# Kernel tuning notes

Measured on AMD Instinct MI355X. Metric: run time of the kernel, lower is better.

The kernel has to match this reference:

```python
import jax, jax.numpy as jnp
import numpy as np

B, S, HID = 2, 2048, 2048
NH, NOPE, ROPE = 16, 128, 64
HD = NOPE + ROPE          # 192
VHD = 128
KVR, QR = 512, 1536
FFN = 5632
THETA = 10000.0
EPS = 1e-6


def rmsnorm(x, w, eps=EPS):
    xf = x.astype(jnp.float32)
    rms = jnp.sqrt(jnp.mean(xf * xf, axis=-1, keepdims=True) + eps)
    return (xf / rms).astype(x.dtype) * w


def apply_rope(x, cos, sin):
    # x: (..., rope_dim); half-split rotation convention
    half = x.shape[-1] // 2
    x1, x2 = x[..., :half], x[..., half:]
    return jnp.concatenate([x1 * cos - x2 * sin, x2 * cos + x1 * sin], axis=-1)


def rope_tables(seq_len, dim, theta=THETA):
    inv_freq = 1.0 / (theta ** (jnp.arange(0, dim, 2, dtype=jnp.float32) / dim))
    t = jnp.arange(seq_len, dtype=jnp.float32)
    freqs = jnp.outer(t, inv_freq)           # (S, dim/2)
    return jnp.cos(freqs), jnp.sin(freqs)


def setup_inputs():
    key = jax.random.key(0)
    ks = jax.random.split(key, 10)
    def w(k, shape, fan_in):
        return jax.random.normal(k, shape, dtype=jnp.float32) * (fan_in ** -0.5)
    return {
        'x': jax.random.normal(ks[0], (B, S, HID), dtype=jnp.float32),
        'attn_norm_w': jnp.ones((HID,), jnp.float32),
        'wq_down': w(ks[1], (HID, QR), HID),
        'wq_up': w(ks[2], (QR, NH * HD), QR),
        'wkv_down': w(ks[3], (HID, KVR + ROPE), HID),
        'kv_norm_w': jnp.ones((KVR,), jnp.float32),
        'wkv_up': w(ks[4], (KVR, NH * (NOPE + VHD)), KVR),
        'wout': w(ks[5], (NH * VHD, HID), NH * VHD),
        'ffn_norm_w': jnp.ones((HID,), jnp.float32),
        'w_gate': w(ks[6], (HID, FFN), HID),
        'w_up': w(ks[7], (HID, FFN), HID),
        'w_down': w(ks[8], (FFN, HID), FFN),
    }


def reference(x, attn_norm_w, wq_down, wq_up, wkv_down, kv_norm_w, wkv_up, wout,
              ffn_norm_w, w_gate, w_up, w_down):
    scale = 1.0 / np.sqrt(HD)
    # --- attention sub-block ---
    h = rmsnorm(x, attn_norm_w)
    q = (h @ wq_down) @ wq_up                       # (B,S,NH*HD)
    q = q.reshape(B, S, NH, HD)
    q_nope, q_rope = q[..., :NOPE], q[..., NOPE:]
    kv_full = h @ wkv_down                          # (B,S,KVR+ROPE)
    kv_c, k_rope = kv_full[..., :KVR], kv_full[..., KVR:]
    kv_c = rmsnorm(kv_c, kv_norm_w)
    kv_exp = (kv_c @ wkv_up).reshape(B, S, NH, NOPE + VHD)
    k_nope, v = kv_exp[..., :NOPE], kv_exp[..., NOPE:]

    cos, sin = rope_tables(S, ROPE)                 # (S, ROPE/2)
    cos4, sin4 = cos[None, :, None, :], sin[None, :, None, :]
    q_rope = apply_rope(q_rope, cos4, sin4)         # (B,S,NH,ROPE)
    k_rope = apply_rope(k_rope[:, :, None, :], cos4, sin4)  # (B,S,1,ROPE)
    k_rope = jnp.broadcast_to(k_rope, (B, S, NH, ROPE))

    q_full = jnp.concatenate([q_nope, q_rope], axis=-1)     # (B,S,NH,HD)
    k = jnp.concatenate([k_nope, k_rope], axis=-1)          # (B,S,NH,HD)

    scores = jnp.einsum('bqhd,bkhd->bhqk', q_full, k) * scale
    causal = jnp.tril(jnp.ones((S, S), dtype=bool))
    scores = jnp.where(causal[None, None], scores, jnp.finfo(scores.dtype).min)
    probs = jax.nn.softmax(scores, axis=-1)
    attn = jnp.einsum('bhqk,bkhd->bqhd', probs, v).reshape(B, S, NH * VHD)
    x = x + attn @ wout

    # --- SwiGLU MLP sub-block ---
    h2 = rmsnorm(x, ffn_norm_w)
    ffn = (jax.nn.silu(h2 @ w_gate) * (h2 @ w_up)) @ w_down
    return x + ffn
```

## Files before the change

### kernel.cpp

```cpp
#include <hip/hip_runtime.h>
#include <hip/hip_bf16.h>


using bf16x8 = __attribute__((ext_vector_type(8))) short;
using f32x4  = __attribute__((ext_vector_type(4))) float;

#define GLOBAL_AS __attribute__((address_space(1)))
#define LDS_AS    __attribute__((address_space(3)))
#define MFMA16(a, b, c) __builtin_amdgcn_mfma_f32_16x16x32_bf16((a), (b), (c), 0, 0, 0)

static constexpr int Sc = 2048;

__device__ __forceinline__ void gload16(const void* g, void* l) {
  __builtin_amdgcn_global_load_lds((const GLOBAL_AS unsigned int*)g,
                                   (LDS_AS unsigned int*)l, 16, 0, 0);
}
__device__ __forceinline__ float bf2f(unsigned short u) {
  union { float f; unsigned int i; } x; x.i = ((unsigned int)u) << 16; return x.f;
}
__device__ __forceinline__ unsigned short f2bf(float f) {
  union { float f; unsigned int i; } x; x.f = f;
  unsigned int i = x.i;
  return (unsigned short)((i + 0x7fffu + ((i >> 16) & 1u)) >> 16);
}
__device__ __forceinline__ int swz4(int r) { return ((r >> 2) & 3) ^ (r & 3); }

__global__ void fill_k(float* out, float v, int n) {
  int i = blockIdx.x * 256 + threadIdx.x;
  if (i < n) out[i] = v;
}

__global__ __launch_bounds__(256) void wtrans(const float* __restrict__ W,
                                              unsigned short* __restrict__ WT,
                                              int K, int N) {
  __shared__ float t[32][33];
  const int n0 = blockIdx.x * 32, k0 = blockIdx.y * 32;
  const int tx = threadIdx.x & 31, ty = threadIdx.x >> 5;
#pragma unroll
  for (int i = 0; i < 4; ++i) {
    int k = k0 + ty + i * 8;
    int n = n0 + tx;
    t[ty + i * 8][tx] = (n < N) ? W[(size_t)k * N + n] : 0.0f;
  }
  __syncthreads();
#pragma unroll
  for (int i = 0; i < 4; ++i) {
    int n = n0 + ty + i * 8;
    int k = k0 + tx;
    WT[(size_t)n * K + k] = f2bf(t[tx][ty + i * 8]);
  }
}

__global__ void rope_tab(float* __restrict__ cosT, float* __restrict__ sinT) {
  int i = blockIdx.x * 256 + threadIdx.x;
  if (i >= Sc * 32) return;
  int s = i >> 5, j = i & 31;
  float inv = powf(10000.0f, -(float)j / 32.0f);
  float a = (float)s * inv;
  cosT[i] = cosf(a);
  sinT[i] = sinf(a);
}

__global__ __launch_bounds__(256) void rmsnorm_k(const float* __restrict__ in,
                                                 const float* __restrict__ w,
                                                 unsigned short* __restrict__ out,
                                                 int D, int istride, int ostride) {
  const int row = blockIdx.x;
  const float* x = in + (size_t)row * istride;
  float ss = 0.f;
  for (int c = threadIdx.x * 4; c < D; c += 1024) {
    const float4 v = *(const float4*)(x + c);
    ss += v.x * v.x + v.y * v.y + v.z * v.z + v.w * v.w;
  }
#pragma unroll
  for (int off = 1; off < 64; off <<= 1) ss += __shfl_xor(ss, off);
  __shared__ float part[4];
  if ((threadIdx.x & 63) == 0) part[threadIdx.x >> 6] = ss;
  __syncthreads();
  float tot = part[0] + part[1] + part[2] + part[3];
  float r = rsqrtf(tot / (float)D + 1e-6f);
  for (int c = threadIdx.x * 4; c < D; c += 1024) {
    const float4 v = *(const float4*)(x + c);
    ushort4 o;
    o.x = f2bf(v.x * r * w[c + 0]);
    o.y = f2bf(v.y * r * w[c + 1]);
    o.z = f2bf(v.z * r * w[c + 2]);
    o.w = f2bf(v.w * r * w[c + 3]);
    *(ushort4*)(out + (size_t)row * ostride + c) = o;
  }
}

enum { EPI_BF16 = 0, EPI_F32 = 1, EPI_ADDF32 = 2, EPI_SILU = 3 };

template <int BMW, int EPI>
__global__ __launch_bounds__(512, 2) void gemm_big(const unsigned short* __restrict__ A,
                                                   const unsigned short* __restrict__ BT,
                                                   void* __restrict__ Cp,
                                                   const float* __restrict__ resid,
                                                   const unsigned short* __restrict__ other,
                                                   int M, int N, int K) {
  constexpr int BM = 128 * BMW;
  constexpr int AL = 2 * BMW;
  constexpr int MF = 4 * BMW;
  __shared__ unsigned short ldsA[2][BM * 64];
  __shared__ unsigned short ldsB[2][256 * 64];

  const int tid = threadIdx.x;
  const int w = tid >> 6, lane = tid & 63;
  const int rl = lane & 15, gh = lane >> 4;
  const int wm = w >> 2, wn = w & 3;

  const int nwg = gridDim.x;
  const int orig = blockIdx.x;
  const int qq = nwg >> 3, rr = nwg & 7;
  const int xcd = orig & 7, lidx = orig >> 3;
  const int fswz = (xcd < rr ? xcd * (qq + 1) : rr * (qq + 1) + (xcd - rr) * qq) + lidx;
  const int MT = M / BM;
  const int m0 = (fswz % MT) * BM;
  const int n0 = (fswz / MT) * 256;

  const unsigned short* srcA[AL];
#pragma unroll
  for (int i = 0; i < AL; ++i) {
    int G = i * 512 + tid, r = G >> 3, sl = (G & 7) ^ (r & 7);
    srcA[i] = A + (size_t)(m0 + r) * K + sl * 8;
  }
  const unsigned short* srcB[4];
#pragma unroll
  for (int i = 0; i < 4; ++i) {
    int G = i * 512 + tid, r = G >> 3, sl = (G & 7) ^ (r & 7);
    srcB[i] = BT + (size_t)(n0 + r) * K + sl * 8;
  }

  auto STAGE = [&](int kt, int p) {
    const int ko = kt * 64;
#pragma unroll
    for (int i = 0; i < AL; ++i)
      gload16(srcA[i] + ko, &ldsA[p][(i * 512 + w * 64) * 8]);
#pragma unroll
    for (int i = 0; i < 4; ++i)
      gload16(srcB[i] + ko, &ldsB[p][(i * 512 + w * 64) * 8]);
  };

  f32x4 acc[MF][4] = {};
  const int nk = K >> 6;

  STAGE(0, 0);
  STAGE(1, 1);
  if constexpr (BMW == 2) asm volatile("s_waitcnt vmcnt(8)" ::: "memory");
  else                    asm volatile("s_waitcnt vmcnt(6)" ::: "memory");
  __builtin_amdgcn_s_barrier();
  __builtin_amdgcn_sched_barrier(0);

  for (int kt = 0; kt < nk; ++kt) {
    const int cur = kt & 1;
    const unsigned short* lA = &ldsA[cur][0];
    const unsigned short* lB = &ldsB[cur][0];
    bf16x8 a[MF][2], b[4][2];
#pragma unroll
    for (int mf = 0; mf < MF; ++mf)
#pragma unroll
      for (int ks = 0; ks < 2; ++ks) {
        const int row = wm * (64 * BMW) + mf * 16 + rl;
        a[mf][ks] = *(const bf16x8*)&lA[row * 64 + (((ks << 2) + gh) ^ (row & 7)) * 8];
      }
#pragma unroll
    for (int nf = 0; nf < 4; ++nf)
#pragma unroll
      for (int ks = 0; ks < 2; ++ks) {
        const int row = wn * 64 + nf * 16 + rl;
        b[nf][ks] = *(const bf16x8*)&lB[row * 64 + (((ks << 2) + gh) ^ (row & 7)) * 8];
      }
    asm volatile("s_waitcnt lgkmcnt(0)" ::: "memory");
    __builtin_amdgcn_sched_barrier(0);
    __builtin_amdgcn_s_barrier();
    __builtin_amdgcn_sched_barrier(0);
    STAGE((kt + 2 < nk) ? kt + 2 : kt, cur);
    __builtin_amdgcn_s_setprio(1);
#pragma unroll
    for (int ks = 0; ks < 2; ++ks)
#pragma unroll
      for (int mf = 0; mf < MF; ++mf)
#pragma unroll
        for (int nf = 0; nf < 4; ++nf)
          acc[mf][nf] = MFMA16(a[mf][ks], b[nf][ks], acc[mf][nf]);
    __builtin_amdgcn_s_setprio(0);
    __builtin_amdgcn_sched_barrier(0);
    if constexpr (BMW == 2) asm volatile("s_waitcnt vmcnt(8)" ::: "memory");
    else                    asm volatile("s_waitcnt vmcnt(6)" ::: "memory");
    __builtin_amdgcn_s_barrier();
    __builtin_amdgcn_sched_barrier(0);
  }

#pragma unroll
  for (int mf = 0; mf < MF; ++mf) {
#pragma unroll
    for (int nf = 0; nf < 4; ++nf) {
#pragma unroll
      for (int rg = 0; rg < 4; ++rg) {
        const int row = m0 + wm * (64 * BMW) + mf * 16 + gh * 4 + rg;
        const int col = n0 + wn * 64 + nf * 16 + rl;
        const size_t idx = (size_t)row * N + col;
        const float v = acc[mf][nf][rg];
        if constexpr (EPI == EPI_BF16) {
          ((unsigned short*)Cp)[idx] = f2bf(v);
        } else if constexpr (EPI == EPI_F32) {
          ((float*)Cp)[idx] = v;
        } else if constexpr (EPI == EPI_ADDF32) {
          ((float*)Cp)[idx] = v + resid[idx];
        } else {
          float gv = bf2f(other[idx]);
          float sg = gv / (1.f + __expf(-gv));
          ((unsigned short*)Cp)[idx] = f2bf(sg * v);
        }
      }
    }
  }
}

template <int EPI>
__global__ __launch_bounds__(256) void gemm_bt(const unsigned short* __restrict__ A,
                                               const unsigned short* __restrict__ BT,
                                               void* __restrict__ Cp,
                                               const float* __restrict__ resid,
                                               const unsigned short* __restrict__ other,
                                               int M, int N, int K) {
  __shared__ unsigned short ldsA[2][128 * 32];
  __shared__ unsigned short ldsB[2][128 * 32];
  const int tid = threadIdx.x;
  const int w = tid >> 6, lane = tid & 63;
  const int nwg = gridDim.x;
  const int orig = blockIdx.x;
  const int qq = nwg >> 3, rr = nwg & 7;
  const int xcd = orig & 7, lidx = orig >> 3;
  const int fswz = (xcd < rr ? xcd * (qq + 1) : rr * (qq + 1) + (xcd - rr) * qq) + lidx;
  const int m0 = (fswz & 31) * 128;
  const int n0 = (fswz >> 5) * 128;

  const int wm = (w >> 1) * 64, wn = (w & 1) * 64;
  const int rl = lane & 15, gsel = lane >> 4;

  const int p0 = w * 64 + lane;
  const int p1 = p0 + 256;
  const int r0 = p0 >> 2, r1 = p1 >> 2;
  const int g0 = (p0 & 3) ^ swz4(r0), g1 = (p1 & 3) ^ swz4(r1);
  const unsigned short* gA0 = A + (size_t)(m0 + r0) * K + g0 * 8;
  const unsigned short* gA1 = A + (size_t)(m0 + r1) * K + g1 * 8;
  const unsigned short* gB0 = BT + (size_t)(n0 + r0) * K + g0 * 8;
  const unsigned short* gB1 = BT + (size_t)(n0 + r1) * K + g1 * 8;
  const int dA0 = (w * 64) * 8, dA1 = dA0 + 2048;

  int aoff[4], boff[4];
#pragma unroll
  for (int i = 0; i < 4; ++i) {
    int ra = wm + i * 16 + rl;
    aoff[i] = ra * 32 + (gsel ^ swz4(ra)) * 8;
    int rb = wn + i * 16 + rl;
    boff[i] = rb * 32 + (gsel ^ swz4(rb)) * 8;
  }

  auto STAGE = [&](int kt, int p) {
    const int ko = kt * 32;
    gload16(gA0 + ko, &ldsA[p][dA0]);
    gload16(gA1 + ko, &ldsA[p][dA1]);
    gload16(gB0 + ko, &ldsB[p][dA0]);
    gload16(gB1 + ko, &ldsB[p][dA1]);
  };

  f32x4 acc[4][4] = {};
  const int nk = K >> 5;

  STAGE(0, 0);
  STAGE(1, 1);
  for (int kt = 0; kt < nk; ++kt) {
    asm volatile("s_waitcnt vmcnt(4)" ::: "memory");
    __builtin_amdgcn_s_barrier();
    __builtin_amdgcn_sched_barrier(0);
    const unsigned short* lA = &ldsA[kt & 1][0];
    const unsigned short* lB = &ldsB[kt & 1][0];
    bf16x8 a[4], b[4];
#pragma unroll
    for (int i = 0; i < 4; ++i) a[i] = *(const bf16x8*)&lA[aoff[i]];
#pragma unroll
    for (int i = 0; i < 4; ++i) b[i] = *(const bf16x8*)&lB[boff[i]];
    __builtin_amdgcn_s_setprio(1);
#pragma unroll
    for (int i = 0; i < 4; ++i)
#pragma unroll
      for (int j = 0; j < 4; ++j) acc[i][j] = MFMA16(a[i], b[j], acc[i][j]);
    __builtin_amdgcn_s_setprio(0);
    __builtin_amdgcn_sched_barrier(0);
    __builtin_amdgcn_s_barrier();
    const int nxt = (kt + 2 < nk) ? kt + 2 : nk - 1;
    STAGE(nxt, kt & 1);
  }

#pragma unroll
  for (int i = 0; i < 4; ++i) {
#pragma unroll
    for (int j = 0; j < 4; ++j) {
#pragma unroll
      for (int rg = 0; rg < 4; ++rg) {
        const int row = m0 + wm + i * 16 + gsel * 4 + rg;
        const int col = n0 + wn + j * 16 + rl;
        const size_t idx = (size_t)row * N + col;
        const float v = acc[i][j][rg];
        if constexpr (EPI == EPI_BF16) {
          ((unsigned short*)Cp)[idx] = f2bf(v);
        } else if constexpr (EPI == EPI_F32) {
          ((float*)Cp)[idx] = v;
        } else if constexpr (EPI == EPI_ADDF32) {
          ((float*)Cp)[idx] = v + resid[idx];
        } else {
          float gv = bf2f(other[idx]);
          float sg = gv / (1.f + __expf(-gv));
          ((unsigned short*)Cp)[idx] = f2bf(sg * v);
        }
      }
    }
  }
}

__global__ __launch_bounds__(256) void repack_q(const unsigned short* __restrict__ q,
                                                const float* __restrict__ cosT,
                                                const float* __restrict__ sinT,
                                                unsigned short* __restrict__ Qc) {
  const int row = blockIdx.x;
  const int b = row >> 11, s = row & 2047;
  const float scale = 0.07216878364870322f;
  const unsigned short* qr = q + (size_t)row * 3072;
  for (int i = threadIdx.x; i < 3072; i += 256) {
    int h = i / 192, d = i - h * 192;
    float v;
    if (d < 128) {
      v = bf2f(qr[h * 192 + d]);
    } else {
      int j = d - 128;
      int jj = j & 31;
      float x1 = bf2f(qr[h * 192 + 128 + jj]);
      float x2 = bf2f(qr[h * 192 + 160 + jj]);
      float c = cosT[s * 32 + jj], sn = sinT[s * 32 + jj];
      v = (j < 32) ? (x1 * c - x2 * sn) : (x2 * c + x1 * sn);
    }
    Qc[((size_t)(b * 16 + h) * Sc + s) * 192 + d] = f2bf(v * scale);
  }
}

__global__ __launch_bounds__(256) void repack_kv(const unsigned short* __restrict__ kvex,
                                                 const float* __restrict__ kvf,
                                                 const float* __restrict__ cosT,
                                                 const float* __restrict__ sinT,
                                                 unsigned short* __restrict__ Kc,
                                                 unsigned short* __restrict__ VT) {
  __shared__ unsigned short vt_lds[32][136];
  const int bid = blockIdx.x;
  const int st = bid & 63;
  const int h = (bid >> 6) & 15;
  const int b = bid >> 10;
  const int s0 = st * 32;
  const int tid = threadIdx.x;
  const size_t KcBase = (size_t)(b * 16 + h) * Sc;
  for (int i = tid; i < 32 * 32; i += 256) {
    int r = i >> 5, g = i & 31;
    uint4 vdat = *(const uint4*)(kvex + (size_t)(b * Sc + s0 + r) * 4096 + h * 256 + g * 8);
    if (g < 16) {
      *(uint4*)(Kc + (KcBase + s0 + r) * 192 + g * 8) = vdat;
    } else {
      *(uint4*)(&vt_lds[r][(g - 16) * 8]) = vdat;
    }
  }
  for (int i = tid; i < 32 * 64; i += 256) {
    int r = i >> 6, d = i & 63;
    int s = s0 + r;
    int jj = d & 31;
    const float* kvrow = kvf + (size_t)(b * Sc + s) * 640;
    float x1 = kvrow[512 + jj], x2 = kvrow[544 + jj];
    float c = cosT[s * 32 + jj], sn = sinT[s * 32 + jj];
    float v = (d < 32) ? (x1 * c - x2 * sn) : (x2 * c + x1 * sn);
    Kc[(KcBase + s) * 192 + 128 + d] = f2bf(v);
  }
  __syncthreads();
  const int f = tid >> 1, sh = (tid & 1) * 16;
  unsigned int vals[8];
#pragma unroll
  for (int k2 = 0; k2 < 8; ++k2) {
    unsigned int lo = vt_lds[sh + 2 * k2][f];
    unsigned int hi = vt_lds[sh + 2 * k2 + 1][f];
    vals[k2] = lo | (hi << 16);
  }
  unsigned short* dst = VT + ((size_t)(b * 16 + h) * 128 + f) * Sc + s0 + sh;
  ((uint4*)dst)[0] = make_uint4(vals[0], vals[1], vals[2], vals[3]);
  ((uint4*)dst)[1] = make_uint4(vals[4], vals[5], vals[6], vals[7]);
}

__global__ __launch_bounds__(256) void attn_k(const unsigned short* __restrict__ Qc,
                                              const unsigned short* __restrict__ Kc,
                                              const unsigned short* __restrict__ VT,
                                              unsigned short* __restrict__ Ob) {
  __shared__ unsigned short lds_k[2][32 * 192];
  __shared__ unsigned short lds_v[2][128 * 32];
  __shared__ __align__(16) unsigned short p_lds[4][16 * 40];
  const int tid = threadIdx.x, w = tid >> 6, lane = tid & 63;
  const int rl = lane & 15, gh = lane >> 4;
  const int bidx = blockIdx.x;
  const int bh = bidx & 31;
  const int qt = 31 - (bidx >> 5);
  const unsigned short* Qh = Qc + (size_t)bh * Sc * 192;
  const unsigned short* Kh = Kc + (size_t)bh * Sc * 192;
  const unsigned short* Vh = VT + (size_t)bh * 128 * Sc;
  const int qr0 = qt * 64 + w * 16;

  bf16x8 qf[6];
#pragma unroll
  for (int kk = 0; kk < 6; ++kk)
    qf[kk] = *(const bf16x8*)(Qh + (size_t)(qr0 + rl) * 192 + kk * 32 + gh * 8);

  f32x4 o[8] = {};
  float mrun[4] = {-1e30f, -1e30f, -1e30f, -1e30f};
  float srun[4] = {0.f, 0.f, 0.f, 0.f};

  int kr[3], kg[3];
#pragma unroll
  for (int j = 0; j < 3; ++j) {
    int pp = j * 256 + w * 64 + lane;
    int r = pp / 24, gq = pp - r * 24;
    kr[j] = r;
    kg[j] = (gq & ~7) | ((gq & 7) ^ (r & 7));
  }
  int vr[2], vg[2];
#pragma unroll
  for (int j = 0; j < 2; ++j) {
    int pp = j * 256 + w * 64 + lane;
    int r = pp >> 2;
    vr[j] = r;
    vg[j] = (pp & 3) ^ swz4(r);
  }

  auto STAGE = [&](int t, int b) {
    const int k0 = t * 32;
#pragma unroll
    for (int j = 0; j < 3; ++j)
      gload16(Kh + (size_t)(k0 + kr[j]) * 192 + kg[j] * 8,
              &lds_k[b][(j * 256 + w * 64) * 8]);
#pragma unroll
    for (int j = 0; j < 2; ++j)
      gload16(Vh + (size_t)vr[j] * Sc + k0 + vg[j] * 8,
              &lds_v[b][(j * 256 + w * 64) * 8]);
  };

  STAGE(0, 0);
  asm volatile("s_waitcnt vmcnt(0)" ::: "memory");
  __builtin_amdgcn_s_barrier();
  __builtin_amdgcn_sched_barrier(0);

  const int nt = 2 * qt + 2;
  int cur = 0;
  for (int t = 0; t < nt; ++t) {
    if (t + 1 < nt) STAGE(t + 1, cur ^ 1);
    const int k0 = t * 32;
    if (k0 <= qr0 + 15) {
      const unsigned short* lk = lds_k[cur];
      const unsigned short* lv = lds_v[cur];
      f32x4 s0 = {0.f, 0.f, 0.f, 0.f}, s1 = {0.f, 0.f, 0.f, 0.f};
      __builtin_amdgcn_s_setprio(1);
#pragma unroll
      for (int kk = 0; kk < 6; ++kk) {
        const int gq = kk * 4 + gh;
        const int ph0 = (gq & ~7) | ((gq & 7) ^ (rl & 7));
        bf16x8 kf0 = *(const bf16x8*)&lk[rl * 192 + ph0 * 8];
        s0 = MFMA16(qf[kk], kf0, s0);
        bf16x8 kf1 = *(const bf16x8*)&lk[(16 + rl) * 192 + ph0 * 8];
        s1 = MFMA16(qf[kk], kf1, s1);
      }
      __builtin_amdgcn_s_setprio(0);
      if (k0 + 31 > qr0) {
#pragma unroll
        for (int rg = 0; rg < 4; ++rg) {
          int qrow = qr0 + gh * 4 + rg;
          if (k0 + rl > qrow) s0[rg] = -1e30f;
          if (k0 + 16 + rl > qrow) s1[rg] = -1e30f;
        }
      }
      float al[4];
#pragma unroll
      for (int rg = 0; rg < 4; ++rg) {
        float v = fmaxf(s0[rg], s1[rg]);
        v = fmaxf(v, __shfl_xor(v, 1));
        v = fmaxf(v, __shfl_xor(v, 2));
        v = fmaxf(v, __shfl_xor(v, 4));
        v = fmaxf(v, __shfl_xor(v, 8));
        float mn = fmaxf(mrun[rg], v);
        al[rg] = __expf(mrun[rg] - mn);
        mrun[rg] = mn;
        float p0 = __expf(s0[rg] - mn), p1 = __expf(s1[rg] - mn);
        s0[rg] = p0;
        s1[rg] = p1;
        float rs = p0 + p1;
        rs += __shfl_xor(rs, 1);
        rs += __shfl_xor(rs, 2);
        rs += __shfl_xor(rs, 4);
        rs += __shfl_xor(rs, 8);
        srun[rg] = srun[rg] * al[rg] + rs;
      }
#pragma unroll
      for (int i = 0; i < 8; ++i)
#pragma unroll
        for (int rg = 0; rg < 4; ++rg) o[i][rg] *= al[rg];
      unsigned short* pw = p_lds[w];
#pragma unroll
      for (int rg = 0; rg < 4; ++rg) {
        pw[(gh * 4 + rg) * 40 + rl] = f2bf(s0[rg]);
        pw[(gh * 4 + rg) * 40 + 16 + rl] = f2bf(s1[rg]);
      }
      bf16x8 pa = *(const bf16x8*)&pw[rl * 40 + gh * 8];
      __builtin_amdgcn_s_setprio(1);
#pragma unroll
      for (int vf = 0; vf < 8; ++vf) {
        int r = vf * 16 + rl;
        bf16x8 vfr = *(const bf16x8*)&lv[r * 32 + (gh ^ swz4(r)) * 8];
        o[vf] = MFMA16(pa, vfr, o[vf]);
      }
      __builtin_amdgcn_s_setprio(0);
    }
    asm volatile("s_waitcnt vmcnt(0)" ::: "memory");
    __builtin_amdgcn_s_barrier();
    __builtin_amdgcn_sched_barrier(0);
    cur ^= 1;
  }
  const int b = bh >> 4, hh = bh & 15;
  float rd[4];
#pragma unroll
  for (int rg = 0; rg < 4; ++rg) rd[rg] = 1.f / srun[rg];
#pragma unroll
  for (int vf = 0; vf < 8; ++vf) {
#pragma unroll
    for (int rg = 0; rg < 4; ++rg) {
      int srow = qr0 + gh * 4 + rg;
      int col = hh * 128 + vf * 16 + rl;
      Ob[((size_t)(b * Sc) + srow) * 2048 + col] = f2bf(o[vf][rg] * rd[rg]);
    }
  }
}

extern "C" void kernel_launch(void* const* d_in, const int* in_sizes, int n_in,
                              void* d_out, int out_size, void* d_ws, size_t ws_size,
                              hipStream_t stream) {
  (void)in_sizes; (void)n_in;
  const float* x    = (const float*)d_in[0];
  const float* anw  = (const float*)d_in[1];
  const float* wqd  = (const float*)d_in[2];
  const float* wqu  = (const float*)d_in[3];
  const float* wkvd = (const float*)d_in[4];
  const float* kvnw = (const float*)d_in[5];
  const float* wkvu = (const float*)d_in[6];
  const float* wout = (const float*)d_in[7];
  const float* fnw  = (const float*)d_in[8];
  const float* wg   = (const float*)d_in[9];
  const float* wu   = (const float*)d_in[10];
  const float* wd   = (const float*)d_in[11];
  float* out = (float*)d_out;

  char* ws = (char*)d_ws;
  size_t off = 0;
  auto alloc = [&](size_t bytes) -> char* {
    char* p = ws + off;
    off += (bytes + 255) & ~(size_t)255;
    return p;
  };
  unsigned short* wslot = (unsigned short*)alloc(5632ull * 2048 * 2);
  float* cosT           = (float*)alloc(2048ull * 32 * 4);
  float* sinT           = (float*)alloc(2048ull * 32 * 4);
  unsigned short* hbuf  = (unsigned short*)alloc(4096ull * 2048 * 2);
  char* arena           = alloc(4096ull * 1536 * 2 + 4096ull * 3072 * 2);
  float* kvf            = (float*)alloc(4096ull * 640 * 4);
  unsigned short* kvn   = (unsigned short*)alloc(4096ull * 512 * 2);
  unsigned short* Qc    = (unsigned short*)alloc(32ull * 2048 * 192 * 2);
  unsigned short* Kc    = (unsigned short*)alloc(32ull * 2048 * 192 * 2);
  unsigned short* VTb   = (unsigned short*)alloc(32ull * 128 * 2048 * 2);
  const size_t NEED = off;

  if (ws_size < NEED) {
    fill_k<<<dim3((out_size + 255) / 256), dim3(256), 0, stream>>>(
        out, (float)(ws_size >> 20), out_size);
    return;
  }

  unsigned short* qd    = (unsigned short*)arena;
  unsigned short* q     = (unsigned short*)(arena + 4096ull * 1536 * 2);
  unsigned short* kvex  = (unsigned short*)arena;
  unsigned short* h     = hbuf;
  unsigned short* attnb = hbuf;
  unsigned short* h2    = hbuf;
  unsigned short* gbuf  = Qc;
  float* x2             = out;

  dim3 blk(256), blk512(512);
  rope_tab<<<dim3(256), blk, 0, stream>>>(cosT, sinT);
  rmsnorm_k<<<dim3(4096), blk, 0, stream>>>(x, anw, h, 2048, 2048, 2048);

  wtrans<<<dim3(48, 64), blk, 0, stream>>>(wqd, wslot, 2048, 1536);
  gemm_big<1, EPI_BF16><<<dim3(32 * 6), blk512, 0, stream>>>(h, wslot, qd, nullptr, nullptr, 4096, 1536, 2048);
  wtrans<<<dim3(96, 48), blk, 0, stream>>>(wqu, wslot, 1536, 3072);
  gemm_big<2, EPI_BF16><<<dim3(16 * 12), blk512, 0, stream>>>(qd, wslot, q, nullptr, nullptr, 4096, 3072, 1536);
  repack_q<<<dim3(4096), blk, 0, stream>>>(q, cosT, sinT, Qc);

  wtrans<<<dim3(20, 64), blk, 0, stream>>>(wkvd, wslot, 2048, 576);
  gemm_bt<EPI_F32><<<dim3(5 * 32), blk, 0, stream>>>(h, wslot, kvf, nullptr, nullptr, 4096, 640, 2048);
  rmsnorm_k<<<dim3(4096), blk, 0, stream>>>(kvf, kvnw, kvn, 512, 640, 512);
  wtrans<<<dim3(128, 16), blk, 0, stream>>>(wkvu, wslot, 512, 4096);
  gemm_big<2, EPI_BF16><<<dim3(16 * 16), blk512, 0, stream>>>(kvn, wslot, kvex, nullptr, nullptr, 4096, 4096, 512);
  repack_kv<<<dim3(2048), blk, 0, stream>>>(kvex, kvf, cosT, sinT, Kc, VTb);

  attn_k<<<dim3(1024), blk, 0, stream>>>(Qc, Kc, VTb, attnb);
  wtrans<<<dim3(64, 64), blk, 0, stream>>>(wout, wslot, 2048, 2048);
  gemm_big<1, EPI_ADDF32><<<dim3(32 * 8), blk512, 0, stream>>>(attnb, wslot, x2, x, nullptr, 4096, 2048, 2048);

  rmsnorm_k<<<dim3(4096), blk, 0, stream>>>(x2, fnw, h2, 2048, 2048, 2048);
  wtrans<<<dim3(176, 64), blk, 0, stream>>>(wg, wslot, 2048, 5632);
  gemm_big<2, EPI_BF16><<<dim3(16 * 22), blk512, 0, stream>>>(h2, wslot, gbuf, nullptr, nullptr, 4096, 5632, 2048);
  wtrans<<<dim3(176, 64), blk, 0, stream>>>(wu, wslot, 2048, 5632);
  gemm_big<2, EPI_SILU><<<dim3(16 * 22), blk512, 0, stream>>>(h2, wslot, gbuf, nullptr, gbuf, 4096, 5632, 2048);
  wtrans<<<dim3(64, 176), blk, 0, stream>>>(wd, wslot, 5632, 2048);
  gemm_big<1, EPI_ADDF32><<<dim3(32 * 8), blk512, 0, stream>>>(gbuf, wslot, out, x2, nullptr, 4096, 2048, 5632);
}
```

Measured before the change: 834.0 us.

## Enlarge attention tiles to 128 queries x 64 keys with lazy rescale; widen weight transpose stores

The attention kernel now runs 512 threads per block, covering 128 query rows and streaming 64-key K/V tiles with an 8-way XOR swizzle. This halves the number of barriers and staging steps per key and gives more reuse of each loaded K/V tile. Online softmax skips rescaling of the accumulator unless the new tile max exceeds the running max by more than 8, and the row-sum reduction is deferred to the end. The weight transpose kernel now handles 64 K-rows per block and writes packed pairs of bf16 as 32-bit stores. The bigger tiles raise LDS use, which may reduce occupancy, and the lazy rescale relies on exp staying within fp32/bf16 range.

```diff
diff --git a/kernel.cpp b/kernel.cpp
--- a/kernel.cpp
+++ b/kernel.cpp
@@ -33,11 +33,11 @@
 __global__ __launch_bounds__(256) void wtrans(const float* __restrict__ W,
                                               unsigned short* __restrict__ WT,
                                               int K, int N) {
-  __shared__ float t[32][33];
-  const int n0 = blockIdx.x * 32, k0 = blockIdx.y * 32;
+  __shared__ float t[64][33];
+  const int n0 = blockIdx.x * 32, k0 = blockIdx.y * 64;
   const int tx = threadIdx.x & 31, ty = threadIdx.x >> 5;
 #pragma unroll
-  for (int i = 0; i < 4; ++i) {
+  for (int i = 0; i < 8; ++i) {
     int k = k0 + ty + i * 8;
     int n = n0 + tx;
     t[ty + i * 8][tx] = (n < N) ? W[(size_t)k * N + n] : 0.0f;
@@ -45,9 +45,11 @@
   __syncthreads();
 #pragma unroll
   for (int i = 0; i < 4; ++i) {
-    int n = n0 + ty + i * 8;
-    int k = k0 + tx;
-    WT[(size_t)n * K + k] = f2bf(t[tx][ty + i * 8]);
+    int nl = ty + i * 8;
+    int kp = tx;
+    unsigned int lo = f2bf(t[kp * 2][nl]);
+    unsigned int hi = f2bf(t[kp * 2 + 1][nl]);
+    *(unsigned int*)(WT + (size_t)(n0 + nl) * K + k0 + kp * 2) = lo | (hi << 16);
   }
 }
 
@@ -393,22 +395,22 @@
   ((uint4*)dst)[1] = make_uint4(vals[4], vals[5], vals[6], vals[7]);
 }
 
-__global__ __launch_bounds__(256) void attn_k(const unsigned short* __restrict__ Qc,
+__global__ __launch_bounds__(512) void attn_k(const unsigned short* __restrict__ Qc,
                                               const unsigned short* __restrict__ Kc,
                                               const unsigned short* __restrict__ VT,
                                               unsigned short* __restrict__ Ob) {
-  __shared__ unsigned short lds_k[2][32 * 192];
-  __shared__ unsigned short lds_v[2][128 * 32];
-  __shared__ __align__(16) unsigned short p_lds[4][16 * 40];
+  __shared__ unsigned short lds_k[2][64 * 192];
+  __shared__ unsigned short lds_v[2][128 * 64];
+  __shared__ __align__(16) unsigned short p_lds[8][16 * 72];
   const int tid = threadIdx.x, w = tid >> 6, lane = tid & 63;
   const int rl = lane & 15, gh = lane >> 4;
   const int bidx = blockIdx.x;
   const int bh = bidx & 31;
-  const int qt = 31 - (bidx >> 5);
+  const int qt = 15 - (bidx >> 5);
   const unsigned short* Qh = Qc + (size_t)bh * Sc * 192;
   const unsigned short* Kh = Kc + (size_t)bh * Sc * 192;
   const unsigned short* Vh = VT + (size_t)bh * 128 * Sc;
-  const int qr0 = qt * 64 + w * 16;
+  const int qr0 = qt * 128 + w * 16;
 
   bf16x8 qf[6];
 #pragma unroll
@@ -422,30 +424,30 @@
   int kr[3], kg[3];
 #pragma unroll
   for (int j = 0; j < 3; ++j) {
-    int pp = j * 256 + w * 64 + lane;
-    int r = pp / 24, gq = pp - r * 24;
+    int G = j * 512 + tid;
+    int r = G / 24, gq = G - r * 24;
     kr[j] = r;
     kg[j] = (gq & ~7) | ((gq & 7) ^ (r & 7));
   }
   int vr[2], vg[2];
 #pragma unroll
   for (int j = 0; j < 2; ++j) {
-    int pp = j * 256 + w * 64 + lane;
-    int r = pp >> 2;
+    int G = j * 512 + tid;
+    int r = G >> 3;
     vr[j] = r;
-    vg[j] = (pp & 3) ^ swz4(r);
+    vg[j] = (G & 7) ^ (r & 7);
   }
 
   auto STAGE = [&](int t, int b) {
-    const int k0 = t * 32;
+    const int k0 = t * 64;
 #pragma unroll
     for (int j = 0; j < 3; ++j)
       gload16(Kh + (size_t)(k0 + kr[j]) * 192 + kg[j] * 8,
-              &lds_k[b][(j * 256 + w * 64) * 8]);
+              &lds_k[b][(j * 512 + w * 64) * 8]);
 #pragma unroll
     for (int j = 0; j < 2; ++j)
       gload16(Vh + (size_t)vr[j] * Sc + k0 + vg[j] * 8,
-              &lds_v[b][(j * 256 + w * 64) * 8]);
+              &lds_v[b][(j * 512 + w * 64) * 8]);
   };
 
   STAGE(0, 0);
@@ -457,68 +459,78 @@
   int cur = 0;
   for (int t = 0; t < nt; ++t) {
     if (t + 1 < nt) STAGE(t + 1, cur ^ 1);
-    const int k0 = t * 32;
+    const int k0 = t * 64;
     if (k0 <= qr0 + 15) {
       const unsigned short* lk = lds_k[cur];
       const unsigned short* lv = lds_v[cur];
-      f32x4 s0 = {0.f, 0.f, 0.f, 0.f}, s1 = {0.f, 0.f, 0.f, 0.f};
+      f32x4 s[4] = {};
       __builtin_amdgcn_s_setprio(1);
 #pragma unroll
       for (int kk = 0; kk < 6; ++kk) {
         const int gq = kk * 4 + gh;
-        const int ph0 = (gq & ~7) | ((gq & 7) ^ (rl & 7));
-        bf16x8 kf0 = *(const bf16x8*)&lk[rl * 192 + ph0 * 8];
-        s0 = MFMA16(qf[kk], kf0, s0);
-        bf16x8 kf1 = *(const bf16x8*)&lk[(16 + rl) * 192 + ph0 * 8];
-        s1 = MFMA16(qf[kk], kf1, s1);
+#pragma unroll
+        for (int ks = 0; ks < 4; ++ks) {
+          const int krow = ks * 16 + rl;
+          const int ph = (gq & ~7) | ((gq & 7) ^ (krow & 7));
+          bf16x8 kf = *(const bf16x8*)&lk[krow * 192 + ph * 8];
+          s[ks] = MFMA16(qf[kk], kf, s[ks]);
+        }
       }
       __builtin_amdgcn_s_setprio(0);
-      if (k0 + 31 > qr0) {
-#pragma unroll
-        for (int rg = 0; rg < 4; ++rg) {
-          int qrow = qr0 + gh * 4 + rg;
-          if (k0 + rl > qrow) s0[rg] = -1e30f;
-          if (k0 + 16 + rl > qrow) s1[rg] = -1e30f;
-        }
-      }
-      float al[4];
+      if (k0 + 63 > qr0) {
+#pragma unroll
+        for (int ks = 0; ks < 4; ++ks)
+#pragma unroll
+          for (int rg = 0; rg < 4; ++rg) {
+            int qrow = qr0 + gh * 4 + rg;
+            if (k0 + ks * 16 + rl > qrow) s[ks][rg] = -1e30f;
+          }
+      }
+      float tmax[4];
 #pragma unroll
       for (int rg = 0; rg < 4; ++rg) {
-        float v = fmaxf(s0[rg], s1[rg]);
+        float v = fmaxf(fmaxf(s[0][rg], s[1][rg]), fmaxf(s[2][rg], s[3][rg]));
         v = fmaxf(v, __shfl_xor(v, 1));
         v = fmaxf(v, __shfl_xor(v, 2));
         v = fmaxf(v, __shfl_xor(v, 4));
         v = fmaxf(v, __shfl_xor(v, 8));
-        float mn = fmaxf(mrun[rg], v);
-        al[rg] = __expf(mrun[rg] - mn);
-        mrun[rg] = mn;
-        float p0 = __expf(s0[rg] - mn), p1 = __expf(s1[rg] - mn);
-        s0[rg] = p0;
-        s1[rg] = p1;
-        float rs = p0 + p1;
-        rs += __shfl_xor(rs, 1);
-        rs += __shfl_xor(rs, 2);
-        rs += __shfl_xor(rs, 4);
-        rs += __shfl_xor(rs, 8);
-        srun[rg] = srun[rg] * al[rg] + rs;
-      }
-#pragma unroll
-      for (int i = 0; i < 8; ++i)
-#pragma unroll
-        for (int rg = 0; rg < 4; ++rg) o[i][rg] *= al[rg];
+        tmax[rg] = v;
+      }
+      int need = !(tmax[0] <= mrun[0] + 8.f && tmax[1] <= mrun[1] + 8.f &&
+                   tmax[2] <= mrun[2] + 8.f && tmax[3] <= mrun[3] + 8.f);
+      if (__any(need)) {
+        float al[4];
+#pragma unroll
+        for (int rg = 0; rg < 4; ++rg) {
+          float mn = fmaxf(mrun[rg], tmax[rg]);
+          al[rg] = __expf(mrun[rg] - mn);
+          mrun[rg] = mn;
+          srun[rg] *= al[rg];
+        }
+#pragma unroll
+        for (int i = 0; i < 8; ++i)
+#pragma unroll
+          for (int rg = 0; rg < 4; ++rg) o[i][rg] *= al[rg];
+      }
       unsigned short* pw = p_lds[w];
 #pragma unroll
-      for (int rg = 0; rg < 4; ++rg) {
-        pw[(gh * 4 + rg) * 40 + rl] = f2bf(s0[rg]);
-        pw[(gh * 4 + rg) * 40 + 16 + rl] = f2bf(s1[rg]);
-      }
-      bf16x8 pa = *(const bf16x8*)&pw[rl * 40 + gh * 8];
+      for (int ks = 0; ks < 4; ++ks)
+#pragma unroll
+        for (int rg = 0; rg < 4; ++rg) {
+          float p = __expf(s[ks][rg] - mrun[rg]);
+          srun[rg] += p;
+          pw[(gh * 4 + rg) * 72 + ks * 16 + rl] = f2bf(p);
+        }
+      bf16x8 pa0 = *(const bf16x8*)&pw[rl * 72 + 0 * 32 + gh * 8];
+      bf16x8 pa1 = *(const bf16x8*)&pw[rl * 72 + 1 * 32 + gh * 8];
       __builtin_amdgcn_s_setprio(1);
 #pragma unroll
       for (int vf = 0; vf < 8; ++vf) {
-        int r = vf * 16 + rl;
-        bf16x8 vfr = *(const bf16x8*)&lv[r * 32 + (gh ^ swz4(r)) * 8];
-        o[vf] = MFMA16(pa, vfr, o[vf]);
+        const int row = vf * 16 + rl;
+        bf16x8 v0 = *(const bf16x8*)&lv[row * 64 + ((0 * 4 + gh) ^ (row & 7)) * 8];
+        o[vf] = MFMA16(pa0, v0, o[vf]);
+        bf16x8 v1 = *(const bf16x8*)&lv[row * 64 + ((1 * 4 + gh) ^ (row & 7)) * 8];
+        o[vf] = MFMA16(pa1, v1, o[vf]);
       }
       __builtin_amdgcn_s_setprio(0);
     }
@@ -527,10 +539,17 @@
     __builtin_amdgcn_sched_barrier(0);
     cur ^= 1;
   }
+  float rd[4];
+#pragma unroll
+  for (int rg = 0; rg < 4; ++rg) {
+    float rs = srun[rg];
+    rs += __shfl_xor(rs, 1);
+    rs += __shfl_xor(rs, 2);
+    rs += __shfl_xor(rs, 4);
+    rs += __shfl_xor(rs, 8);
+    rd[rg] = 1.f / rs;
+  }
   const int b = bh >> 4, hh = bh & 15;
-  float rd[4];
-#pragma unroll
-  for (int rg = 0; rg < 4; ++rg) rd[rg] = 1.f / srun[rg];
 #pragma unroll
   for (int vf = 0; vf < 8; ++vf) {
 #pragma unroll
@@ -598,28 +617,28 @@
   rope_tab<<<dim3(256), blk, 0, stream>>>(cosT, sinT);
   rmsnorm_k<<<dim3(4096), blk, 0, stream>>>(x, anw, h, 2048, 2048, 2048);
 
-  wtrans<<<dim3(48, 64), blk, 0, stream>>>(wqd, wslot, 2048, 1536);
+  wtrans<<<dim3(48, 32), blk, 0, stream>>>(wqd, wslot, 2048, 1536);
   gemm_big<1, EPI_BF16><<<dim3(32 * 6), blk512, 0, stream>>>(h, wslot, qd, nullptr, nullptr, 4096, 1536, 2048);
-  wtrans<<<dim3(96, 48), blk, 0, stream>>>(wqu, wslot, 1536, 3072);
+  wtrans<<<dim3(96, 24), blk, 0, stream>>>(wqu, wslot, 1536, 3072);
   gemm_big<2, EPI_BF16><<<dim3(16 * 12), blk512, 0, stream>>>(qd, wslot, q, nullptr, nullptr, 4096, 3072, 1536);
   repack_q<<<dim3(4096), blk, 0, stream>>>(q, cosT, sinT, Qc);
 
-  wtrans<<<dim3(20, 64), blk, 0, stream>>>(wkvd, wslot, 2048, 576);
+  wtrans<<<dim3(20, 32), blk, 0, stream>>>(wkvd, wslot, 2048, 576);
   gemm_bt<EPI_F32><<<dim3(5 * 32), blk, 0, stream>>>(h, wslot, kvf, nullptr, nullptr, 4096, 640, 2048);
   rmsnorm_k<<<dim3(4096), blk, 0, stream>>>(kvf, kvnw, kvn, 512, 640, 512);
-  wtrans<<<dim3(128, 16), blk, 0, stream>>>(wkvu, wslot, 512, 4096);
+  wtrans<<<dim3(128, 8), blk, 0, stream>>>(wkvu, wslot, 512, 4096);
   gemm_big<2, EPI_BF16><<<dim3(16 * 16), blk512, 0, stream>>>(kvn, wslot, kvex, nullptr, nullptr, 4096, 4096, 512);
   repack_kv<<<dim3(2048), blk, 0, stream>>>(kvex, kvf, cosT, sinT, Kc, VTb);
 
-  attn_k<<<dim3(1024), blk, 0, stream>>>(Qc, Kc, VTb, attnb);
-  wtrans<<<dim3(64, 64), blk, 0, stream>>>(wout, wslot, 2048, 2048);
+  attn_k<<<dim3(512), blk512, 0, stream>>>(Qc, Kc, VTb, attnb);
+  wtrans<<<dim3(64, 32), blk, 0, stream>>>(wout, wslot, 2048, 2048);
   gemm_big<1, EPI_ADDF32><<<dim3(32 * 8), blk512, 0, stream>>>(attnb, wslot, x2, x, nullptr, 4096, 2048, 2048);
 
   rmsnorm_k<<<dim3(4096), blk, 0, stream>>>(x2, fnw, h2, 2048, 2048, 2048);
-  wtrans<<<dim3(176, 64), blk, 0, stream>>>(wg, wslot, 2048, 5632);
+  wtrans<<<dim3(176, 32), blk, 0, stream>>>(wg, wslot, 2048, 5632);
   gemm_big<2, EPI_BF16><<<dim3(16 * 22), blk512, 0, stream>>>(h2, wslot, gbuf, nullptr, nullptr, 4096, 5632, 2048);
-  wtrans<<<dim3(176, 64), blk, 0, stream>>>(wu, wslot, 2048, 5632);
+  wtrans<<<dim3(176, 32), blk, 0, stream>>>(wu, wslot, 2048, 5632);
   gemm_big<2, EPI_SILU><<<dim3(16 * 22), blk512, 0, stream>>>(h2, wslot, gbuf, nullptr, gbuf, 4096, 5632, 2048);
-  wtrans<<<dim3(64, 176), blk, 0, stream>>>(wd, wslot, 5632, 2048);
+  wtrans<<<dim3(64, 88), blk, 0, stream>>>(wd, wslot, 5632, 2048);
   gemm_big<1, EPI_ADDF32><<<dim3(32 * 8), blk512, 0, stream>>>(gbuf, wslot, out, x2, nullptr, 4096, 2048, 5632);
 }
```

Result: faster. 796.6 us (-4.5%).
